# Kernel tuning notes

Measured on AMD Instinct MI355X. Metric: run time of the kernel, lower is better.

The kernel has to match this reference:

```python
import jax, jax.numpy as jnp
import numpy as np

N_NODES = 50000


def gcn_conv(x, W, b, src, dst, n_nodes):
    """PyG GCNConv: h = x @ W; add self-loops; symmetric norm; scatter-add; + bias."""
    h = x @ W  # [N, out]
    loop = jnp.arange(n_nodes, dtype=src.dtype)
    s = jnp.concatenate([src, loop])  # source nodes j
    d = jnp.concatenate([dst, loop])  # target nodes i
    deg = jax.ops.segment_sum(jnp.ones_like(d, dtype=h.dtype), d, num_segments=n_nodes)
    dinv = jnp.where(deg > 0, jax.lax.rsqrt(deg), 0.0)
    norm = dinv[s] * dinv[d]  # [E+N]
    msg = h[s] * norm[:, None]  # gather + scale, [E+N, out]
    out = jax.ops.segment_sum(msg, d, num_segments=n_nodes)
    return out + b


def setup_inputs() -> dict:
    key = jax.random.key(0)
    k1, k2, k3, k4 = jax.random.split(key, 4)
    x = jax.random.normal(k1, (N_NODES, 256), dtype=jnp.float32)
    edge_index = jax.random.randint(k2, (2, 1600000), 0, N_NODES, dtype=jnp.int64)
    in_dim, hid, out_dim = 256, 128, 40
    W1 = jax.random.normal(k3, (in_dim, hid), dtype=jnp.float32) / np.sqrt(in_dim)
    b1 = jnp.zeros((hid,), dtype=jnp.float32)
    W2 = jax.random.normal(k4, (hid, out_dim), dtype=jnp.float32) / np.sqrt(hid)
    b2 = jnp.zeros((out_dim,), dtype=jnp.float32)
    return {"x": x, "edge_index": edge_index, "W1": W1, "b1": b1, "W2": W2, "b2": b2}


def reference(x, edge_index, W1, b1, W2, b2):
    src, dst = edge_index[0], edge_index[1]
    n = x.shape[0]
    h = jax.nn.relu(gcn_conv(x, W1, b1, src, dst, n))
    # dropout is identity in eval mode
    h = gcn_conv(h, W2, b2, src, dst, n)
    return jax.nn.log_softmax(h, axis=1)
```

## Files before the change

kernel.cpp:

```cpp
#include <hip/hip_runtime.h>
#include <cmath>

#define NN 50000
#define C_IN 256
#define C_HID 128
#define C_OUT 40

#define BSZ 512
#define NBUCK ((NN + BSZ - 1) / BSZ)
#define CAP 19456
#define EPB 4096

typedef __attribute__((ext_vector_type(8))) short bf16x8;
typedef __attribute__((ext_vector_type(4))) float f32x4;
typedef __attribute__((ext_vector_type(2))) float f32x2;

__device__ __forceinline__ float bf2f(unsigned int u16) {
  unsigned int b = (u16 & 0xFFFFu) << 16;
  return __builtin_bit_cast(float, b);
}
__device__ __forceinline__ unsigned short f2bf(float f) {
  unsigned int b = __builtin_bit_cast(unsigned int, f);
  unsigned int r = (b + 0x7FFF + ((b >> 16) & 1)) >> 16;
  return (unsigned short)r;
}


__global__ __launch_bounds__(256) void prep_passA_kernel(const float* __restrict__ W1,
    const float* __restrict__ W2, const float* __restrict__ b1,
    uint4* __restrict__ pbuf1, uint4* __restrict__ pbuf2, float* __restrict__ bperm,
    const int* __restrict__ src, const int* __restrict__ dst, int E,
    unsigned int* __restrict__ gedge, int* __restrict__ bcur) {
  __shared__ unsigned int pk[EPB];
  __shared__ unsigned char bof[EPB];
  __shared__ int bcnt[NBUCK], bstart[NBUCK], bpos[NBUCK], gbase[NBUCK];
  int blk = blockIdx.x;
  int tid = threadIdx.x;
  if (blk < 16) {
    int gid = blk * 256 + tid;
    int l = gid & 63, idx = gid >> 6;
    int ks = idx & 7, t = idx >> 3;
    int c = t * 16 + (l & 15);
    int kbase = ks * 32 + (l >> 4) * 8;
    unsigned int u[4];
    #pragma unroll
    for (int jp = 0; jp < 4; ++jp) {
      float v0 = W1[(size_t)(kbase + 2 * jp) * C_HID + c];
      float v1 = W1[(size_t)(kbase + 2 * jp + 1) * C_HID + c];
      u[jp] = (unsigned int)f2bf(v0) | ((unsigned int)f2bf(v1) << 16);
    }
    pbuf1[idx * 64 + l] = make_uint4(u[0], u[1], u[2], u[3]);
    return;
  } else if (blk < 19) {
    int gid = (blk - 16) * 256 + tid;
    int l = gid & 63, idx = gid >> 6;
    int ks = idx & 3, t = idx >> 2;
    int c = t * 16 + (l & 15);
    int kbase = ks * 32 + (l >> 4) * 8;
    unsigned int u[4];
    #pragma unroll
    for (int jp = 0; jp < 4; ++jp) {
      int k0 = kbase + 2 * jp, k1 = k0 + 1;
      int ch0 = ((k0 & 7) << 4) + (k0 >> 3);
      int ch1 = ((k1 & 7) << 4) + (k1 >> 3);
      float v0 = (c < C_OUT) ? W2[(size_t)ch0 * C_OUT + c] : 0.f;
      float v1 = (c < C_OUT) ? W2[(size_t)ch1 * C_OUT + c] : 0.f;
      u[jp] = (unsigned int)f2bf(v0) | ((unsigned int)f2bf(v1) << 16);
    }
    pbuf2[idx * 64 + l] = make_uint4(u[0], u[1], u[2], u[3]);
    return;
  } else if (blk == 19) {
    if (tid < C_HID) bperm[tid] = b1[((tid & 7) << 4) + (tid >> 3)];
    return;
  }
  int e0 = (blk - 20) * EPB;
  int cntE = min(EPB, E - e0);
  for (int b = tid; b < NBUCK; b += 256) bcnt[b] = 0;
  int ds_[16], ss_[16];
  __syncthreads();
  #pragma unroll
  for (int k = 0; k < 16; ++k) {
    int i = tid + k * 256;
    if (i < cntE) {
      ds_[k] = dst[e0 + i];
      ss_[k] = src[e0 + i];
      atomicAdd(&bcnt[ds_[k] >> 9], 1);
    }
  }
  __syncthreads();
  if (tid == 0) {
    int acc = 0;
    for (int b = 0; b < NBUCK; ++b) { bstart[b] = acc; bpos[b] = acc; acc += bcnt[b]; }
  }
  __syncthreads();
  #pragma unroll
  for (int k = 0; k < 16; ++k) {
    int i = tid + k * 256;
    if (i < cntE) {
      int b = ds_[k] >> 9;
      int p = atomicAdd(&bpos[b], 1);
      pk[p] = ((unsigned int)ss_[k] << 9) | (unsigned int)(ds_[k] & 511);
      bof[p] = (unsigned char)b;
    }
  }
  __syncthreads();
  for (int b = tid; b < NBUCK; b += 256)
    gbase[b] = atomicAdd(&bcur[b], bcnt[b]);
  __syncthreads();
  for (int i = tid; i < cntE; i += 256) {
    int b = bof[i];
    int p = gbase[b] + (i - bstart[b]);
    gedge[(size_t)b * CAP + p] = pk[i];
  }
}


__global__ __launch_bounds__(512) void passB_g1_kernel(const unsigned int* __restrict__ gedge,
    const int* __restrict__ bcur, int* __restrict__ esrc, int* __restrict__ off,
    float* __restrict__ dinv, int E,
    const float* __restrict__ x, const uint4* __restrict__ pb, uint2* __restrict__ h) {
  __shared__ int dcnt[512];
  __shared__ int dsc[512];
  __shared__ int dcur[512];
  __shared__ int bc[128];
  int tid = threadIdx.x;
  if ((int)blockIdx.x >= NBUCK) {
    int l = tid & 63, w = tid >> 6;
    int row0 = (blockIdx.x - NBUCK) * 128 + w * 16;
    int arow = min(row0 + (l & 15), NN - 1);
    const float* xp = x + (size_t)arow * C_IN + (l >> 4) * 8;
    bf16x8 a[8];
    #pragma unroll
    for (int ks = 0; ks < 8; ++ks) {
      float4 a0 = *(const float4*)(xp + ks * 32);
      float4 a1 = *(const float4*)(xp + ks * 32 + 4);
      union { bf16x8 v; unsigned short s[8]; } pa;
      pa.s[0] = f2bf(a0.x); pa.s[1] = f2bf(a0.y); pa.s[2] = f2bf(a0.z); pa.s[3] = f2bf(a0.w);
      pa.s[4] = f2bf(a1.x); pa.s[5] = f2bf(a1.y); pa.s[6] = f2bf(a1.z); pa.s[7] = f2bf(a1.w);
      a[ks] = pa.v;
    }
    f32x4 acc[8] = {};
    #pragma unroll
    for (int t = 0; t < 8; ++t) {
      #pragma unroll
      for (int ks = 0; ks < 8; ++ks) {
        bf16x8 b = __builtin_bit_cast(bf16x8, pb[(t * 8 + ks) * 64 + l]);
        acc[t] = __builtin_amdgcn_mfma_f32_16x16x32_bf16(a[ks], b, acc[t], 0, 0, 0);
      }
    }
    int c0 = l & 15, rb = (l >> 4) * 4;
    #pragma unroll
    for (int r = 0; r < 4; ++r) {
      int row = row0 + rb + r;
      if (row < NN) {
        int w0 = __builtin_amdgcn_cvt_pk_fp8_f32(acc[0][r], acc[1][r], 0, false);
        w0     = __builtin_amdgcn_cvt_pk_fp8_f32(acc[2][r], acc[3][r], w0, true);
        int w1 = __builtin_amdgcn_cvt_pk_fp8_f32(acc[4][r], acc[5][r], 0, false);
        w1     = __builtin_amdgcn_cvt_pk_fp8_f32(acc[6][r], acc[7][r], w1, true);
        h[(size_t)row * 16 + c0] = make_uint2((unsigned int)w0, (unsigned int)w1);
      }
    }
    return;
  }
  int b = blockIdx.x;
  int nE = bcur[b];
  if (tid < 128) bc[tid] = (tid < b) ? bcur[tid] : 0;
  dcnt[tid] = 0;
  __syncthreads();
  const unsigned int* reg = gedge + (size_t)b * CAP;
  for (int i = tid; i < nE; i += 512)
    atomicAdd(&dcnt[reg[i] & 511], 1);
  __syncthreads();
  for (int d = 64; d > 0; d >>= 1) {
    if (tid < d) bc[tid] += bc[tid + d];
    __syncthreads();
  }
  int base = bc[0];
  int own = dcnt[tid];
  dsc[tid] = own;
  __syncthreads();
  for (int d = 1; d < 512; d <<= 1) {
    int x_ = (tid >= d) ? dsc[tid - d] : 0;
    __syncthreads();
    dsc[tid] += x_;
    __syncthreads();
  }
  int excl = dsc[tid] - own;
  dcur[tid] = excl;
  int node = b * BSZ + tid;
  if (node < NN) {
    off[node]  = base + excl;
    dinv[node] = rsqrtf((float)(own + 1));
  }
  if (b == 0 && tid == 0) off[NN] = E;
  __syncthreads();
  for (int i = tid; i < nE; i += 512) {
    unsigned int p = reg[i];
    int pos = atomicAdd(&dcur[p & 511], 1);
    esrc[base + pos] = (int)(p >> 9);
  }
}


__global__ __launch_bounds__(256) void gemm2_kernel(const unsigned short* __restrict__ ag1b,
    const uint4* __restrict__ pbuf, unsigned char* __restrict__ h2) {
  int l = threadIdx.x & 63, w = threadIdx.x >> 6;
  int row0 = blockIdx.x * 64 + w * 16;
  int arow = min(row0 + (l & 15), NN - 1);
  const uint4* ap = (const uint4*)(ag1b + (size_t)arow * C_HID + (l >> 4) * 8);
  bf16x8 a[4];
  #pragma unroll
  for (int ks = 0; ks < 4; ++ks) a[ks] = __builtin_bit_cast(bf16x8, ap[ks * 4]);
  f32x4 acc[3] = {};
  #pragma unroll
  for (int t = 0; t < 3; ++t) {
    #pragma unroll
    for (int ks = 0; ks < 4; ++ks) {
      bf16x8 b = __builtin_bit_cast(bf16x8, pbuf[(t * 4 + ks) * 64 + l]);
      acc[t] = __builtin_amdgcn_mfma_f32_16x16x32_bf16(a[ks], b, acc[t], 0, 0, 0);
    }
  }
  int rbase = row0 + (l >> 4) * 4;
  int c0 = l & 15;
  #pragma unroll
  for (int t = 0; t < 3; ++t) {
    int col = t * 16 + c0;
    if (col < C_OUT) {
      #pragma unroll
      for (int r = 0; r < 4; ++r) {
        int row = rbase + r;
        if (row < NN) {
          int pk = __builtin_amdgcn_cvt_pk_fp8_f32(acc[t][r], 0.f, 0, false);
          h2[(size_t)row * C_OUT + col] = (unsigned char)(pk & 0xFF);
        }
      }
    }
  }
}


__global__ void agg1_kernel(const uint4* __restrict__ h, const int* __restrict__ off,
                            const int* __restrict__ esrc, const float* __restrict__ dinv,
                            const float* __restrict__ bperm, uint4* __restrict__ outb,
                            int n, int E) {
  int wv = threadIdx.x >> 6, l = threadIdx.x & 63;
  int i = blockIdx.x * 4 + wv;
  if (i >= n) return;
  int g = l >> 3, j = l & 7;
  float di = dinv[i];
  float a[16];
  #pragma unroll
  for (int k = 0; k < 16; ++k) a[k] = 0.f;
  int p0 = off[i], p1 = off[i + 1];
  int pb = p0;
  int Em1 = E - 1;
  int sA0 = esrc[min(pb + g, Em1)];
  int sB0 = esrc[min(pb + 8 + g, Em1)];
  int sA1 = esrc[min(pb + 16 + g, Em1)];
  int sB1 = esrc[min(pb + 24 + g, Em1)];
  uint4 HA = h[(size_t)sA0 * 8 + j];
  uint4 HB = h[(size_t)sB0 * 8 + j];
  float nA = dinv[sA0];
  float nB = dinv[sB0];
  #define ACC_E(vv, nn)                                                       \
    {                                                                         \
      float n_ = (nn) * di;                                                   \
      f32x2 p0_ = __builtin_amdgcn_cvt_pk_f32_fp8((int)vv.x, false);          \
      f32x2 p1_ = __builtin_amdgcn_cvt_pk_f32_fp8((int)vv.x, true);           \
      f32x2 p2_ = __builtin_amdgcn_cvt_pk_f32_fp8((int)vv.y, false);          \
      f32x2 p3_ = __builtin_amdgcn_cvt_pk_f32_fp8((int)vv.y, true);           \
      f32x2 p4_ = __builtin_amdgcn_cvt_pk_f32_fp8((int)vv.z, false);          \
      f32x2 p5_ = __builtin_amdgcn_cvt_pk_f32_fp8((int)vv.z, true);           \
      f32x2 p6_ = __builtin_amdgcn_cvt_pk_f32_fp8((int)vv.w, false);          \
      f32x2 p7_ = __builtin_amdgcn_cvt_pk_f32_fp8((int)vv.w, true);           \
      a[0] += p0_[0] * n_;  a[1] += p0_[1] * n_;                              \
      a[2] += p1_[0] * n_;  a[3] += p1_[1] * n_;                              \
      a[4] += p2_[0] * n_;  a[5] += p2_[1] * n_;                              \
      a[6] += p3_[0] * n_;  a[7] += p3_[1] * n_;                              \
      a[8] += p4_[0] * n_;  a[9] += p4_[1] * n_;                              \
      a[10] += p5_[0] * n_; a[11] += p5_[1] * n_;                             \
      a[12] += p6_[0] * n_; a[13] += p6_[1] * n_;                             \
      a[14] += p7_[0] * n_; a[15] += p7_[1] * n_;                             \
    }
  for (; pb + 31 < p1; pb += 16) {
    uint4 GA = h[(size_t)sA1 * 8 + j];
    uint4 GB = h[(size_t)sB1 * 8 + j];
    float mA = dinv[sA1];
    float mB = dinv[sB1];
    int tA = esrc[min(pb + 32 + g, Em1)];
    int tB = esrc[min(pb + 40 + g, Em1)];
    ACC_E(HA, nA); ACC_E(HB, nB);
    HA = GA; HB = GB; nA = mA; nB = mB;
    sA1 = tA; sB1 = tB;
  }
  if (pb + g < p1)     ACC_E(HA, nA);
  if (pb + 8 + g < p1) ACC_E(HB, nB);
  int pc = pb + 16;
  if (pc < p1) {
    uint4 GA = h[(size_t)sA1 * 8 + j];
    uint4 GB = h[(size_t)sB1 * 8 + j];
    float mA = dinv[sA1];
    float mB = dinv[sB1];
    if (pc + g < p1)     ACC_E(GA, mA);
    if (pc + 8 + g < p1) ACC_E(GB, mB);
  }
  #undef ACC_E
  #pragma unroll
  for (int k = 0; k < 16; ++k) {
    a[k] += __shfl_xor(a[k], 8);
    a[k] += __shfl_xor(a[k], 16);
    a[k] += __shfl_xor(a[k], 32);
  }
  if (g == 0) {
    uint4 sv = h[(size_t)i * 8 + j];
    float dd = di * di;
    f32x2 s0 = __builtin_amdgcn_cvt_pk_f32_fp8((int)sv.x, false);
    f32x2 s1 = __builtin_amdgcn_cvt_pk_f32_fp8((int)sv.x, true);
    f32x2 s2 = __builtin_amdgcn_cvt_pk_f32_fp8((int)sv.y, false);
    f32x2 s3 = __builtin_amdgcn_cvt_pk_f32_fp8((int)sv.y, true);
    f32x2 s4 = __builtin_amdgcn_cvt_pk_f32_fp8((int)sv.z, false);
    f32x2 s5 = __builtin_amdgcn_cvt_pk_f32_fp8((int)sv.z, true);
    f32x2 s6 = __builtin_amdgcn_cvt_pk_f32_fp8((int)sv.w, false);
    f32x2 s7 = __builtin_amdgcn_cvt_pk_f32_fp8((int)sv.w, true);
    a[0] += s0[0] * dd;  a[1] += s0[1] * dd;
    a[2] += s1[0] * dd;  a[3] += s1[1] * dd;
    a[4] += s2[0] * dd;  a[5] += s2[1] * dd;
    a[6] += s3[0] * dd;  a[7] += s3[1] * dd;
    a[8] += s4[0] * dd;  a[9] += s4[1] * dd;
    a[10] += s5[0] * dd; a[11] += s5[1] * dd;
    a[12] += s6[0] * dd; a[13] += s6[1] * dd;
    a[14] += s7[0] * dd; a[15] += s7[1] * dd;
    const float4* bp = (const float4*)bperm + j * 4;
    #pragma unroll
    for (int m = 0; m < 4; ++m) {
      float4 bb = bp[m];
      a[m * 4 + 0] = fmaxf(a[m * 4 + 0] + bb.x, 0.f);
      a[m * 4 + 1] = fmaxf(a[m * 4 + 1] + bb.y, 0.f);
      a[m * 4 + 2] = fmaxf(a[m * 4 + 2] + bb.z, 0.f);
      a[m * 4 + 3] = fmaxf(a[m * 4 + 3] + bb.w, 0.f);
    }
    unsigned int o[8];
    #pragma unroll
    for (int m = 0; m < 8; ++m)
      o[m] = (unsigned int)f2bf(a[2 * m]) | ((unsigned int)f2bf(a[2 * m + 1]) << 16);
    outb[(size_t)i * 16 + j * 2]     = make_uint4(o[0], o[1], o[2], o[3]);
    outb[(size_t)i * 16 + j * 2 + 1] = make_uint4(o[4], o[5], o[6], o[7]);
  }
}

__global__ void agg2_kernel(const unsigned char* __restrict__ h2, const int* __restrict__ off,
                            const int* __restrict__ esrc, const float* __restrict__ dinv,
                            const float* __restrict__ b, float* __restrict__ out,
                            int n, int E) {
  int wv = threadIdx.x >> 6, l = threadIdx.x & 63;
  int i = blockIdx.x * 4 + wv;
  if (i >= n) return;
  int g = l / 10, q = l - g * 10;
  bool lact = l < 60;
  if (!lact) { g = 0; q = 0; }
  float di = dinv[i];
  float a0 = 0.f, a1 = 0.f, a2 = 0.f, a3 = 0.f;
  int p0 = off[i], p1 = off[i + 1];
  int pb = p0;
  int Em1 = E - 1;
  int sA0 = esrc[min(pb + g, Em1)];
  int sB0 = esrc[min(pb + 6 + g, Em1)];
  int sA1 = esrc[min(pb + 12 + g, Em1)];
  int sB1 = esrc[min(pb + 18 + g, Em1)];
  unsigned int HA = *(const unsigned int*)(h2 + (size_t)sA0 * C_OUT + q * 4);
  unsigned int HB = *(const unsigned int*)(h2 + (size_t)sB0 * C_OUT + q * 4);
  float nA = dinv[sA0];
  float nB = dinv[sB0];
  #define ACC_E2(vv, nn)                                                      \
    {                                                                         \
      float n_ = (nn) * di;                                                   \
      f32x2 lo_ = __builtin_amdgcn_cvt_pk_f32_fp8((int)(vv), false);          \
      f32x2 hi_ = __builtin_amdgcn_cvt_pk_f32_fp8((int)(vv), true);           \
      a0 += lo_[0] * n_; a1 += lo_[1] * n_;                                   \
      a2 += hi_[0] * n_; a3 += hi_[1] * n_;                                   \
    }
  for (; pb + 23 < p1; pb += 12) {
    unsigned int GA = *(const unsigned int*)(h2 + (size_t)sA1 * C_OUT + q * 4);
    unsigned int GB = *(const unsigned int*)(h2 + (size_t)sB1 * C_OUT + q * 4);
    float mA = dinv[sA1];
    float mB = dinv[sB1];
    int tA = esrc[min(pb + 24 + g, Em1)];
    int tB = esrc[min(pb + 30 + g, Em1)];
    if (lact) { ACC_E2(HA, nA); ACC_E2(HB, nB); }
    HA = GA; HB = GB; nA = mA; nB = mB;
    sA1 = tA; sB1 = tB;
  }
  if (lact && pb + g < p1)     ACC_E2(HA, nA);
  if (lact && pb + 6 + g < p1) ACC_E2(HB, nB);
  int pc = pb + 12;
  if (pc < p1) {
    unsigned int GA = *(const unsigned int*)(h2 + (size_t)sA1 * C_OUT + q * 4);
    unsigned int GB = *(const unsigned int*)(h2 + (size_t)sB1 * C_OUT + q * 4);
    float mA = dinv[sA1];
    float mB = dinv[sB1];
    if (lact && pc + g < p1)     ACC_E2(GA, mA);
    if (lact && pc + 6 + g < p1) ACC_E2(GB, mB);
  }
  #undef ACC_E2
  float t0 = 0.f, t1 = 0.f, t2 = 0.f, t3 = 0.f;
  #pragma unroll
  for (int gg = 0; gg < 6; ++gg) {
    int sl = gg * 10 + q;
    t0 += __shfl(a0, sl); t1 += __shfl(a1, sl);
    t2 += __shfl(a2, sl); t3 += __shfl(a3, sl);
  }
  bool act = l < 10;
  float v0, v1, v2, v3;
  if (act) {
    unsigned int sv = *(const unsigned int*)(h2 + (size_t)i * C_OUT + l * 4);
    f32x2 slo = __builtin_amdgcn_cvt_pk_f32_fp8((int)sv, false);
    f32x2 shi = __builtin_amdgcn_cvt_pk_f32_fp8((int)sv, true);
    float dd = di * di;
    float4 bb = ((const float4*)b)[l];
    v0 = t0 + slo[0] * dd + bb.x;
    v1 = t1 + slo[1] * dd + bb.y;
    v2 = t2 + shi[0] * dd + bb.z;
    v3 = t3 + shi[1] * dd + bb.w;
  } else {
    v0 = v1 = v2 = v3 = -INFINITY;
  }
  float mm = fmaxf(fmaxf(v0, v1), fmaxf(v2, v3));
  #pragma unroll
  for (int d = 32; d > 0; d >>= 1) mm = fmaxf(mm, __shfl_xor(mm, d));
  float e = act ? (expf(v0 - mm) + expf(v1 - mm) + expf(v2 - mm) + expf(v3 - mm)) : 0.f;
  float ss = e;
  #pragma unroll
  for (int d = 32; d > 0; d >>= 1) ss += __shfl_xor(ss, d);
  if (act) {
    float lg = logf(ss);
    float4 o = {v0 - mm - lg, v1 - mm - lg, v2 - mm - lg, v3 - mm - lg};
    *(float4*)&out[(size_t)i * C_OUT + l * 4] = o;
  }
}


extern "C" void kernel_launch(void* const* d_in, const int* in_sizes, int n_in,
                              void* d_out, int out_size, void* d_ws, size_t ws_size,
                              hipStream_t stream) {
  const float* x  = (const float*)d_in[0];
  const int*   ei = (const int*)d_in[1];
  const float* W1 = (const float*)d_in[2];
  const float* b1 = (const float*)d_in[3];
  const float* W2 = (const float*)d_in[4];
  const float* b2 = (const float*)d_in[5];
  int E = in_sizes[1] / 2;
  const int* src = ei;
  const int* dst = ei + E;

  char* ws = (char*)d_ws;
  size_t o = 0;
  auto alloc = [&](size_t bytes) {
    char* p = ws + o;
    o += (bytes + 255) & ~(size_t)255;
    return p;
  };
  unsigned int* gedge = (unsigned int*)alloc((size_t)NBUCK * CAP * sizeof(unsigned int));
  int*   bcur  = (int*)alloc(NBUCK * sizeof(int));
  int*   off   = (int*)alloc((NN + 1) * sizeof(int));
  float* dinv  = (float*)alloc(NN * sizeof(float));
  int*   esrc  = (int*)alloc((size_t)E * sizeof(int));
  uint2* h1f8  = (uint2*)alloc((size_t)NN * C_HID);
  unsigned int*   ag1b = (unsigned int*)alloc((size_t)NN * (C_HID / 2) * sizeof(unsigned int));
  unsigned char*  h2f8 = (unsigned char*)alloc((size_t)NN * C_OUT);
  uint4* pbuf2 = (uint4*)alloc(12 * 64 * sizeof(uint4));
  uint4* pbuf1 = (uint4*)alloc(64 * 64 * sizeof(uint4));
  float* bperm = (float*)alloc(C_HID * sizeof(float));

  int nA  = (E + EPB - 1) / EPB;
  int ng1 = (NN + 127) / 128;
  int ng2 = (NN + 63) / 64;

  hipMemsetAsync(bcur, 0, NBUCK * sizeof(int), stream);
  prep_passA_kernel<<<20 + nA, 256, 0, stream>>>(W1, W2, b1, pbuf1, pbuf2, bperm,
                                                 src, dst, E, gedge, bcur);
  passB_g1_kernel<<<NBUCK + ng1, 512, 0, stream>>>(gedge, bcur, esrc, off, dinv, E,
                                                   x, pbuf1, h1f8);
  agg1_kernel<<<(NN + 3) / 4, 256, 0, stream>>>((const uint4*)h1f8, off, esrc, dinv,
                                                bperm, (uint4*)ag1b, NN, E);
  gemm2_kernel<<<ng2, 256, 0, stream>>>((const unsigned short*)ag1b, pbuf2, h2f8);
  agg2_kernel<<<(NN + 3) / 4, 256, 0, stream>>>(h2f8, off, esrc, dinv, b2,
                                                (float*)d_out, NN, E);
}
```

Baseline: 130.9 us.

## Fuse layer-1 aggregation with layer-2 GEMM through shared memory

Merges agg1 and gemm2 into one kernel. Each 512-thread block aggregates 8 nodes, writes the bf16 rows into LDS (padded to 16 rows with zeros), then one wave runs the MFMA against W2 and writes fp8 h2. This removes the bf16 ag1b round trip through global memory and one kernel launch. In exchange it adds a block-wide barrier, leaves half of each 16-row MFMA tile as padding, and has only one of eight waves doing the GEMM.

```diff
diff --git a/kernel.cpp b/kernel.cpp
--- a/kernel.cpp
+++ b/kernel.cpp
@@ -202,56 +202,23 @@
 }
 
 
-__global__ __launch_bounds__(256) void gemm2_kernel(const unsigned short* __restrict__ ag1b,
-    const uint4* __restrict__ pbuf, unsigned char* __restrict__ h2) {
-  int l = threadIdx.x & 63, w = threadIdx.x >> 6;
-  int row0 = blockIdx.x * 64 + w * 16;
-  int arow = min(row0 + (l & 15), NN - 1);
-  const uint4* ap = (const uint4*)(ag1b + (size_t)arow * C_HID + (l >> 4) * 8);
-  bf16x8 a[4];
-  #pragma unroll
-  for (int ks = 0; ks < 4; ++ks) a[ks] = __builtin_bit_cast(bf16x8, ap[ks * 4]);
-  f32x4 acc[3] = {};
-  #pragma unroll
-  for (int t = 0; t < 3; ++t) {
-    #pragma unroll
-    for (int ks = 0; ks < 4; ++ks) {
-      bf16x8 b = __builtin_bit_cast(bf16x8, pbuf[(t * 4 + ks) * 64 + l]);
-      acc[t] = __builtin_amdgcn_mfma_f32_16x16x32_bf16(a[ks], b, acc[t], 0, 0, 0);
-    }
-  }
-  int rbase = row0 + (l >> 4) * 4;
-  int c0 = l & 15;
-  #pragma unroll
-  for (int t = 0; t < 3; ++t) {
-    int col = t * 16 + c0;
-    if (col < C_OUT) {
-      #pragma unroll
-      for (int r = 0; r < 4; ++r) {
-        int row = rbase + r;
-        if (row < NN) {
-          int pk = __builtin_amdgcn_cvt_pk_fp8_f32(acc[t][r], 0.f, 0, false);
-          h2[(size_t)row * C_OUT + col] = (unsigned char)(pk & 0xFF);
-        }
-      }
-    }
-  }
-}
-
-
-__global__ void agg1_kernel(const uint4* __restrict__ h, const int* __restrict__ off,
-                            const int* __restrict__ esrc, const float* __restrict__ dinv,
-                            const float* __restrict__ bperm, uint4* __restrict__ outb,
-                            int n, int E) {
-  int wv = threadIdx.x >> 6, l = threadIdx.x & 63;
-  int i = blockIdx.x * 4 + wv;
-  if (i >= n) return;
+__global__ __launch_bounds__(512) void agg1g2_kernel(const uint4* __restrict__ h,
+    const int* __restrict__ off, const int* __restrict__ esrc,
+    const float* __restrict__ dinv, const float* __restrict__ bperm,
+    const uint4* __restrict__ pbuf2, unsigned char* __restrict__ h2, int n, int E) {
+  __shared__ unsigned short rowlds[16][136];
+  int tid = threadIdx.x;
+  int wv = tid >> 6, l = tid & 63;
+  int i = blockIdx.x * 8 + wv;
+  bool nv = i < n;
+  int ii = min(i, n - 1);
   int g = l >> 3, j = l & 7;
-  float di = dinv[i];
+  for (int z = tid; z < 8 * 136; z += 512) rowlds[8 + z / 136][z - (z / 136) * 136] = 0;
+  float di = dinv[ii];
   float a[16];
   #pragma unroll
   for (int k = 0; k < 16; ++k) a[k] = 0.f;
-  int p0 = off[i], p1 = off[i + 1];
+  int p0 = nv ? off[ii] : 0, p1 = nv ? off[ii + 1] : 0;
   int pb = p0;
   int Em1 = E - 1;
   int sA0 = esrc[min(pb + g, Em1)];
@@ -312,39 +279,70 @@
     a[k] += __shfl_xor(a[k], 32);
   }
   if (g == 0) {
-    uint4 sv = h[(size_t)i * 8 + j];
-    float dd = di * di;
-    f32x2 s0 = __builtin_amdgcn_cvt_pk_f32_fp8((int)sv.x, false);
-    f32x2 s1 = __builtin_amdgcn_cvt_pk_f32_fp8((int)sv.x, true);
-    f32x2 s2 = __builtin_amdgcn_cvt_pk_f32_fp8((int)sv.y, false);
-    f32x2 s3 = __builtin_amdgcn_cvt_pk_f32_fp8((int)sv.y, true);
-    f32x2 s4 = __builtin_amdgcn_cvt_pk_f32_fp8((int)sv.z, false);
-    f32x2 s5 = __builtin_amdgcn_cvt_pk_f32_fp8((int)sv.z, true);
-    f32x2 s6 = __builtin_amdgcn_cvt_pk_f32_fp8((int)sv.w, false);
-    f32x2 s7 = __builtin_amdgcn_cvt_pk_f32_fp8((int)sv.w, true);
-    a[0] += s0[0] * dd;  a[1] += s0[1] * dd;
-    a[2] += s1[0] * dd;  a[3] += s1[1] * dd;
-    a[4] += s2[0] * dd;  a[5] += s2[1] * dd;
-    a[6] += s3[0] * dd;  a[7] += s3[1] * dd;
-    a[8] += s4[0] * dd;  a[9] += s4[1] * dd;
-    a[10] += s5[0] * dd; a[11] += s5[1] * dd;
-    a[12] += s6[0] * dd; a[13] += s6[1] * dd;
-    a[14] += s7[0] * dd; a[15] += s7[1] * dd;
-    const float4* bp = (const float4*)bperm + j * 4;
-    #pragma unroll
-    for (int m = 0; m < 4; ++m) {
-      float4 bb = bp[m];
-      a[m * 4 + 0] = fmaxf(a[m * 4 + 0] + bb.x, 0.f);
-      a[m * 4 + 1] = fmaxf(a[m * 4 + 1] + bb.y, 0.f);
-      a[m * 4 + 2] = fmaxf(a[m * 4 + 2] + bb.z, 0.f);
-      a[m * 4 + 3] = fmaxf(a[m * 4 + 3] + bb.w, 0.f);
-    }
-    unsigned int o[8];
-    #pragma unroll
-    for (int m = 0; m < 8; ++m)
-      o[m] = (unsigned int)f2bf(a[2 * m]) | ((unsigned int)f2bf(a[2 * m + 1]) << 16);
-    outb[(size_t)i * 16 + j * 2]     = make_uint4(o[0], o[1], o[2], o[3]);
-    outb[(size_t)i * 16 + j * 2 + 1] = make_uint4(o[4], o[5], o[6], o[7]);
+    float vres[16];
+    if (nv) {
+      uint4 sv = h[(size_t)ii * 8 + j];
+      float dd = di * di;
+      f32x2 s0 = __builtin_amdgcn_cvt_pk_f32_fp8((int)sv.x, false);
+      f32x2 s1 = __builtin_amdgcn_cvt_pk_f32_fp8((int)sv.x, true);
+      f32x2 s2 = __builtin_amdgcn_cvt_pk_f32_fp8((int)sv.y, false);
+      f32x2 s3 = __builtin_amdgcn_cvt_pk_f32_fp8((int)sv.y, true);
+      f32x2 s4 = __builtin_amdgcn_cvt_pk_f32_fp8((int)sv.z, false);
+      f32x2 s5 = __builtin_amdgcn_cvt_pk_f32_fp8((int)sv.z, true);
+      f32x2 s6 = __builtin_amdgcn_cvt_pk_f32_fp8((int)sv.w, false);
+      f32x2 s7 = __builtin_amdgcn_cvt_pk_f32_fp8((int)sv.w, true);
+      a[0] += s0[0] * dd;  a[1] += s0[1] * dd;
+      a[2] += s1[0] * dd;  a[3] += s1[1] * dd;
+      a[4] += s2[0] * dd;  a[5] += s2[1] * dd;
+      a[6] += s3[0] * dd;  a[7] += s3[1] * dd;
+      a[8] += s4[0] * dd;  a[9] += s4[1] * dd;
+      a[10] += s5[0] * dd; a[11] += s5[1] * dd;
+      a[12] += s6[0] * dd; a[13] += s6[1] * dd;
+      a[14] += s7[0] * dd; a[15] += s7[1] * dd;
+      const float4* bp = (const float4*)bperm + j * 4;
+      #pragma unroll
+      for (int m = 0; m < 4; ++m) {
+        float4 bb = bp[m];
+        vres[m * 4 + 0] = fmaxf(a[m * 4 + 0] + bb.x, 0.f);
+        vres[m * 4 + 1] = fmaxf(a[m * 4 + 1] + bb.y, 0.f);
+        vres[m * 4 + 2] = fmaxf(a[m * 4 + 2] + bb.z, 0.f);
+        vres[m * 4 + 3] = fmaxf(a[m * 4 + 3] + bb.w, 0.f);
+      }
+    } else {
+      #pragma unroll
+      for (int m = 0; m < 16; ++m) vres[m] = 0.f;
+    }
+    #pragma unroll
+    for (int m = 0; m < 16; ++m) rowlds[wv][j * 16 + m] = f2bf(vres[m]);
+  }
+  __syncthreads();
+  if (wv == 0) {
+    f32x4 acc[3] = {};
+    #pragma unroll
+    for (int ks = 0; ks < 4; ++ks) {
+      bf16x8 af = *(const bf16x8*)&rowlds[l & 15][ks * 32 + (l >> 4) * 8];
+      #pragma unroll
+      for (int t = 0; t < 3; ++t) {
+        bf16x8 b = __builtin_bit_cast(bf16x8, pbuf2[(t * 4 + ks) * 64 + l]);
+        acc[t] = __builtin_amdgcn_mfma_f32_16x16x32_bf16(af, b, acc[t], 0, 0, 0);
+      }
+    }
+    int c0 = l & 15, rb = l >> 4;
+    #pragma unroll
+    for (int t = 0; t < 3; ++t) {
+      int col = t * 16 + c0;
+      if (col < C_OUT) {
+        #pragma unroll
+        for (int r = 0; r < 4; ++r) {
+          int rowidx = rb * 4 + r;
+          int node = blockIdx.x * 8 + rowidx;
+          if (rowidx < 8 && node < n) {
+            int pk = __builtin_amdgcn_cvt_pk_fp8_f32(acc[t][r], 0.f, 0, false);
+            h2[(size_t)node * C_OUT + col] = (unsigned char)(pk & 0xFF);
+          }
+        }
+      }
+    }
   }
 }
 
@@ -465,7 +463,6 @@
   float* dinv  = (float*)alloc(NN * sizeof(float));
   int*   esrc  = (int*)alloc((size_t)E * sizeof(int));
   uint2* h1f8  = (uint2*)alloc((size_t)NN * C_HID);
-  unsigned int*   ag1b = (unsigned int*)alloc((size_t)NN * (C_HID / 2) * sizeof(unsigned int));
   unsigned char*  h2f8 = (unsigned char*)alloc((size_t)NN * C_OUT);
   uint4* pbuf2 = (uint4*)alloc(12 * 64 * sizeof(uint4));
   uint4* pbuf1 = (uint4*)alloc(64 * 64 * sizeof(uint4));
@@ -473,16 +470,14 @@
 
   int nA  = (E + EPB - 1) / EPB;
   int ng1 = (NN + 127) / 128;
-  int ng2 = (NN + 63) / 64;
 
   hipMemsetAsync(bcur, 0, NBUCK * sizeof(int), stream);
   prep_passA_kernel<<<20 + nA, 256, 0, stream>>>(W1, W2, b1, pbuf1, pbuf2, bperm,
                                                  src, dst, E, gedge, bcur);
   passB_g1_kernel<<<NBUCK + ng1, 512, 0, stream>>>(gedge, bcur, esrc, off, dinv, E,
                                                    x, pbuf1, h1f8);
-  agg1_kernel<<<(NN + 3) / 4, 256, 0, stream>>>((const uint4*)h1f8, off, esrc, dinv,
-                                                bperm, (uint4*)ag1b, NN, E);
-  gemm2_kernel<<<ng2, 256, 0, stream>>>((const unsigned short*)ag1b, pbuf2, h2f8);
+  agg1g2_kernel<<<(NN + 7) / 8, 512, 0, stream>>>((const uint4*)h1f8, off, esrc, dinv,
+                                                  bperm, pbuf2, h2f8, NN, E);
   agg2_kernel<<<(NN + 3) / 4, 256, 0, stream>>>(h2f8, off, esrc, dinv, b2,
                                                 (float*)d_out, NN, E);
 }
```

New measurement: 139.6 us. 1.07x slower.
